# Kernel optimization log

Measured on AMD Instinct MI355X. Metric: run time of the kernel, lower is better.

The kernel has to match this reference:

```python
import jax, jax.numpy as jnp
import numpy as np

N, E = 50000, 800000
IN_C, HID, OUT_C = 100, 128, 40
LAYERS, GROUPS, CODES = 3, 3, 16
BETA = 0.98
EPS = 1e-5


def setup_inputs() -> dict:
    key = jax.random.key(0)
    ks = jax.random.split(key, 16)
    lin = lambda k, i, o: (jax.random.normal(k, (i, o), jnp.float32) / np.sqrt(i)).astype(jnp.float32)
    d = {}
    d["x"] = jax.random.normal(ks[0], (N, IN_C), jnp.float32)
    d["src"] = jax.random.randint(ks[1], (E,), 0, N, jnp.int32)
    d["dst"] = jax.random.randint(ks[2], (E,), 0, N, jnp.int32)
    # SAGEConv params: lin_l (aggregated, with bias) and lin_r (root, no bias)
    d["W0a"], d["W0r"], d["b0"] = lin(ks[3], IN_C, HID), lin(ks[4], IN_C, HID), jnp.zeros((HID,), jnp.float32)
    d["W1a"], d["W1r"], d["b1"] = lin(ks[5], HID, HID), lin(ks[6], HID, HID), jnp.zeros((HID,), jnp.float32)
    d["W2a"], d["W2r"], d["b2"] = lin(ks[7], HID, HID), lin(ks[8], HID, HID), jnp.zeros((HID,), jnp.float32)
    # BatchNorm (eval mode: running stats) for first num_layers-1 = 2 layers
    d["bn_gamma"] = jnp.ones((2, HID), jnp.float32)
    d["bn_beta"] = jnp.zeros((2, HID), jnp.float32)
    d["bn_mean"] = jnp.zeros((2, HID), jnp.float32)
    d["bn_var"] = jnp.ones((2, HID), jnp.float32)
    # Residual VQ codebooks: [layer, group, num_codes, feature]
    d["codebooks"] = 0.1 * jax.random.normal(ks[9], (LAYERS, GROUPS, CODES, HID), jnp.float32)
    d["lin_W"] = lin(ks[10], HID, OUT_C)
    d["lin_b"] = jnp.zeros((OUT_C,), jnp.float32)
    return d


def _sage_conv(h, src, dst, Wa, Wr, b):
    # mean neighbor aggregation (PyG SAGEConv, aggr='mean')
    msg = h[src]                                              # [E, d]
    agg = jax.ops.segment_sum(msg, dst, num_segments=N)       # [N, d]
    deg = jax.ops.segment_sum(jnp.ones((E,), h.dtype), dst, num_segments=N)
    agg = agg / jnp.maximum(deg, 1.0)[:, None]
    return agg @ Wa + b + h @ Wr


def _rvq(h, cb):
    # residual vector quantization over GROUPS codebooks; cb: [G, K, D]
    res, quant, ids = h, jnp.zeros_like(h), []
    for g in range(GROUPS):
        c = cb[g]                                             # [K, D]
        d2 = (jnp.sum(res * res, -1, keepdims=True)
              - 2.0 * res @ c.T + jnp.sum(c * c, -1))          # [N, K]
        idx = jnp.argmin(d2, axis=-1)
        q = c[idx]
        quant = quant + q
        res = res - q
        ids.append(idx)
    sg = jax.lax.stop_gradient
    loss = (BETA * jnp.mean((h - sg(quant)) ** 2)
            + (1.0 - BETA) * jnp.mean((sg(h) - quant) ** 2))
    return loss, jnp.stack(ids, axis=1)                        # [N, G] int


def reference(x, src, dst, W0a, W0r, b0, W1a, W1r, b1, W2a, W2r, b2,
              bn_gamma, bn_beta, bn_mean, bn_var, codebooks, lin_W, lin_b):
    Ws = [(W0a, W0r, b0), (W1a, W1r, b1), (W2a, W2r, b2)]
    h = x
    total_loss = jnp.float32(0.0)
    id_list = []
    for i in range(LAYERS - 1):
        h = _sage_conv(h, src, dst, *Ws[i])
        h = (h - bn_mean[i]) * jax.lax.rsqrt(bn_var[i] + EPS) * bn_gamma[i] + bn_beta[i]
        h = jax.nn.relu(h)                                     # dropout: eval mode (identity)
        loss, ids = _rvq(h, codebooks[i])
        total_loss = total_loss + loss
        id_list.append(ids)
    h = _sage_conv(h, src, dst, *Ws[-1])
    loss, ids = _rvq(h, codebooks[-1])
    total_loss = total_loss + loss
    id_list.append(ids)
    out = h @ lin_W + lin_b
    return out, total_loss, jnp.concatenate(id_list, axis=1)
```

## Files before the change

kernel.cpp:

```cpp
#include <hip/hip_runtime.h>

#define NN 50000
#define HID 128
#define IN_C 100
#define OUT_C 40

__global__ __launch_bounds__(256)
void hist_kernel(const int* __restrict__ dst, int* __restrict__ deg, int E) {
    int e = blockIdx.x * 256 + threadIdx.x;
    if (e < E) atomicAdd(&deg[dst[e]], 1);
}

__global__ __launch_bounds__(256)
void chunk_sum_kernel(const int* __restrict__ deg, int* __restrict__ chunk_sums, int N) {
    __shared__ int s[256];
    const int t = threadIdx.x;
    const int i = blockIdx.x * 256 + t;
    s[t] = (i < N) ? deg[i] : 0;
    __syncthreads();
    for (int o = 128; o; o >>= 1) { if (t < o) s[t] += s[t + o]; __syncthreads(); }
    if (t == 0) chunk_sums[blockIdx.x] = s[0];
}

__global__ __launch_bounds__(256)
void chunk_scan_kernel(int* __restrict__ chunk_sums, int M) {
    __shared__ int s[256];
    const int t = threadIdx.x;
    int v = (t < M) ? chunk_sums[t] : 0;
    s[t] = v;
    __syncthreads();
    for (int o = 1; o < 256; o <<= 1) {
        int x = (t >= o) ? s[t - o] : 0;
        __syncthreads();
        s[t] += x;
        __syncthreads();
    }
    if (t < M) chunk_sums[t] = s[t] - v;
}

__global__ __launch_bounds__(256)
void chunk_apply_kernel(const int* __restrict__ deg, const int* __restrict__ chunk_sums,
                        int* __restrict__ row_start, int* __restrict__ cursor, int N) {
    __shared__ int s[256];
    const int t = threadIdx.x;
    const int i = blockIdx.x * 256 + t;
    int v = (i < N) ? deg[i] : 0;
    s[t] = v;
    __syncthreads();
    for (int o = 1; o < 256; o <<= 1) {
        int x = (t >= o) ? s[t - o] : 0;
        __syncthreads();
        s[t] += x;
        __syncthreads();
    }
    if (i < N) {
        int ex = chunk_sums[blockIdx.x] + s[t] - v;
        row_start[i] = ex;
        cursor[i] = ex;
        if (i == N - 1) row_start[N] = ex + v;
    }
}

__global__ __launch_bounds__(256)
void scatter_kernel(const int* __restrict__ src, const int* __restrict__ dst,
                    int* __restrict__ cursor, int* __restrict__ csr_src, int E) {
    int e = blockIdx.x * 256 + threadIdx.x;
    if (e < E) {
        int pos = atomicAdd(&cursor[dst[e]], 1);
        csr_src[pos] = src[e];
    }
}

__global__ __launch_bounds__(128)
void prep_pack(const float* __restrict__ Wa, const float* __restrict__ Wr,
               float2* __restrict__ wp) {
    const int k = blockIdx.x, col = threadIdx.x;
    float2 v;
    v.x = Wa[(size_t)k * HID + col];
    v.y = Wr[(size_t)k * HID + col];
    wp[(size_t)k * HID + col] = v;
}

template<int K, bool HAS_BN, bool LAST>
__global__ __launch_bounds__(512, 6)
void layer_fused(const float* __restrict__ h_in,
                 const int* __restrict__ row_start, const int* __restrict__ csr_src,
                 const float2* __restrict__ wp, const float* __restrict__ b,
                 const float* __restrict__ gamma, const float* __restrict__ beta,
                 const float* __restrict__ mean, const float* __restrict__ var,
                 const float* __restrict__ cb,
                 float* __restrict__ h_out,
                 float* __restrict__ ids_out, int id_col0,
                 double* __restrict__ loss_part,
                 const float* __restrict__ lin_W, const float* __restrict__ lin_b,
                 float* __restrict__ out) {
    __shared__ double s_agg[8][HID];
    __shared__ double s_h[8][HID];
    __shared__ float s_cb[3 * 16 * HID];
    __shared__ double s_ws[8];
    const int t = threadIdx.x;
    const int w = t >> 6, lane = t & 63;
    const int n0 = blockIdx.x * 8;

    for (int idx = t; idx < 3 * 16 * HID; idx += 512) s_cb[idx] = cb[idx];

    {
        const int n = n0 + w;
        const int r0 = row_start[n], r1 = row_start[n + 1];
        const int f0 = 2 * lane;
        if (f0 < K) {
            double a0 = 0.0, a1 = 0.0, c0 = 0.0, c1 = 0.0;
            int i = r0;
            for (; i + 1 < r1; i += 2) {
                const float2 v0 = *(const float2*)(h_in + (size_t)csr_src[i] * K + f0);
                const float2 v1 = *(const float2*)(h_in + (size_t)csr_src[i + 1] * K + f0);
                a0 += (double)v0.x; a1 += (double)v0.y;
                c0 += (double)v1.x; c1 += (double)v1.y;
            }
            if (i < r1) {
                const float2 v0 = *(const float2*)(h_in + (size_t)csr_src[i] * K + f0);
                a0 += (double)v0.x; a1 += (double)v0.y;
            }
            const int deg = r1 - r0;
            const double dd = (double)(deg > 1 ? deg : 1);
            const float2 root = *(const float2*)(h_in + (size_t)n * K + f0);
            s_agg[w][f0]     = (a0 + c0) / dd;
            s_agg[w][f0 + 1] = (a1 + c1) / dd;
            s_h[w][f0]     = (double)root.x;
            s_h[w][f0 + 1] = (double)root.y;
        }
    }
    __syncthreads();

    const int col = t & 127;
    const int p4 = t >> 7;
    double accA = (double)b[col];
    double accB = accA;
#pragma unroll 4
    for (int k = 0; k < K; ++k) {
        const float2 wv = wp[(size_t)k * HID + col];
        const double wa = (double)wv.x, wr = (double)wv.y;
        accA += s_agg[p4][k] * wa + s_h[p4][k] * wr;
        accB += s_agg[p4 + 4][k] * wa + s_h[p4 + 4][k] * wr;
    }
    __syncthreads();

    {
        double vA = accA, vB = accB;
        if (HAS_BN) {
            const double scale = (double)gamma[col] / sqrt((double)var[col] + 1e-5);
            const double shift = (double)beta[col] - (double)mean[col] * scale;
            vA = vA * scale + shift; vA = vA > 0.0 ? vA : 0.0;
            vB = vB * scale + shift; vB = vB > 0.0 ? vB : 0.0;
        }
        const float fA = (float)vA, fB = (float)vB;
        h_out[(size_t)(n0 + p4) * HID + col] = fA;
        h_out[(size_t)(n0 + p4 + 4) * HID + col] = fB;
        s_agg[p4][col] = (double)fA;
        s_agg[p4 + 4][col] = (double)fB;
        if (LAST) {
            s_h[p4][col] = (double)fA;
            s_h[p4 + 4][col] = (double)fB;
        }
    }
    __syncthreads();

    {
        double* res = &s_agg[w][0];
        const int n = n0 + w;
        const int k = lane & 15, q = lane >> 4;
        const int jbase = q * 32;
        const int rot = (k + 8 * q) & 31;

        for (int g = 0; g < 3; ++g) {
            const float* c = &s_cb[(g * 16 + k) * HID];
            double r0 = res[lane], r1 = res[lane + 64];
            double pr = r0 * r0 + r1 * r1;
            pr += __shfl_xor(pr, 1, 64);
            pr += __shfl_xor(pr, 2, 64);
            pr += __shfl_xor(pr, 4, 64);
            pr += __shfl_xor(pr, 8, 64);
            pr += __shfl_xor(pr, 16, 64);
            pr += __shfl_xor(pr, 32, 64);
            const float rr32 = (float)pr;

            double cc = 0.0, dot = 0.0;
#pragma unroll
            for (int j2 = 0; j2 < 32; ++j2) {
                const int j = jbase + ((j2 + rot) & 31);
                const double cj = (double)c[j];
                cc += cj * cj;
                dot += res[j] * cj;
            }
            cc += __shfl_xor(cc, 16, 64);
            cc += __shfl_xor(cc, 32, 64);
            dot += __shfl_xor(dot, 16, 64);
            dot += __shfl_xor(dot, 32, 64);

            const float cc32 = (float)cc;
            const float rc32 = (float)dot;
            const float t1 = rr32 - 2.0f * rc32;
            const float d2 = t1 + cc32;

            float bv = d2; int bk = k;
            {
                float ov; int ok;
                ov = __shfl_xor(bv, 1, 64); ok = __shfl_xor(bk, 1, 64);
                if (ov < bv || (ov == bv && ok < bk)) { bv = ov; bk = ok; }
                ov = __shfl_xor(bv, 2, 64); ok = __shfl_xor(bk, 2, 64);
                if (ov < bv || (ov == bv && ok < bk)) { bv = ov; bk = ok; }
                ov = __shfl_xor(bv, 4, 64); ok = __shfl_xor(bk, 4, 64);
                if (ov < bv || (ov == bv && ok < bk)) { bv = ov; bk = ok; }
                ov = __shfl_xor(bv, 8, 64); ok = __shfl_xor(bk, 8, 64);
                if (ov < bv || (ov == bv && ok < bk)) { bv = ov; bk = ok; }
            }
            if (lane == 0)
                ids_out[(size_t)n * 9 + id_col0 + g] = (float)bk;

            const float* cbest = &s_cb[(g * 16 + bk) * HID];
            res[lane]      -= (double)cbest[lane];
            res[lane + 64] -= (double)cbest[lane + 64];
        }
        double r0 = res[lane], r1 = res[lane + 64];
        double wl = r0 * r0 + r1 * r1;
        wl += __shfl_xor(wl, 1, 64);
        wl += __shfl_xor(wl, 2, 64);
        wl += __shfl_xor(wl, 4, 64);
        wl += __shfl_xor(wl, 8, 64);
        wl += __shfl_xor(wl, 16, 64);
        wl += __shfl_xor(wl, 32, 64);
        if (lane == 0) s_ws[w] = wl;
    }

    if (LAST) {
        const int n = n0 + w;
        if (lane < OUT_C) {
            double acc = (double)lin_b[lane];
            for (int kk = 0; kk < HID; ++kk)
                acc += s_h[w][kk] * (double)lin_W[kk * OUT_C + lane];
            out[(size_t)n * OUT_C + lane] = (float)acc;
        }
    }

    __syncthreads();
    if (t == 0) {
        double s = 0.0;
#pragma unroll
        for (int i = 0; i < 8; i++) s += s_ws[i];
        loss_part[blockIdx.x] = s;
    }
}

__global__ __launch_bounds__(256)
void finalize_kernel(const double* __restrict__ loss_part, int M,
                     float* __restrict__ out_loss) {
    __shared__ double s[256];
    const int t = threadIdx.x;
    double v = 0.0;
    for (int i = t; i < M; i += 256) v += loss_part[i];
    s[t] = v;
    __syncthreads();
    for (int off = 128; off; off >>= 1) {
        if (t < off) s[t] += s[t + off];
        __syncthreads();
    }
    if (t == 0) out_loss[0] = (float)(s[0] / ((double)NN * (double)HID));
}

extern "C" void kernel_launch(void* const* d_in, const int* in_sizes, int n_in,
                              void* d_out, int out_size, void* d_ws, size_t ws_size,
                              hipStream_t stream) {
    const float* x    = (const float*)d_in[0];
    const int*   src  = (const int*)d_in[1];
    const int*   dst  = (const int*)d_in[2];
    const float* W0a = (const float*)d_in[3];
    const float* W0r = (const float*)d_in[4];
    const float* b0  = (const float*)d_in[5];
    const float* W1a = (const float*)d_in[6];
    const float* W1r = (const float*)d_in[7];
    const float* b1  = (const float*)d_in[8];
    const float* W2a = (const float*)d_in[9];
    const float* W2r = (const float*)d_in[10];
    const float* b2  = (const float*)d_in[11];
    const float* bn_gamma = (const float*)d_in[12];
    const float* bn_beta  = (const float*)d_in[13];
    const float* bn_mean  = (const float*)d_in[14];
    const float* bn_var   = (const float*)d_in[15];
    const float* cb    = (const float*)d_in[16];
    const float* lin_W = (const float*)d_in[17];
    const float* lin_b = (const float*)d_in[18];

    const int E = in_sizes[1];

    float* out      = (float*)d_out;
    float* out_loss = out + (size_t)NN * OUT_C;
    float* out_ids  = out_loss + 1;

    char* base = (char*)d_ws;
    size_t off = 0;
    auto alloc = [&](size_t bytes) -> void* {
        off = (off + 511) & ~(size_t)511;
        void* p = base + off;
        off += bytes;
        return p;
    };
    int* deg_i      = (int*)alloc((size_t)NN * 4);
    int* row_start  = (int*)alloc((size_t)(NN + 1) * 4);
    int* cursor     = (int*)alloc((size_t)NN * 4);
    int* csr_src    = (int*)alloc((size_t)E * 4);
    int* chunk_sums = (int*)alloc(256 * 4);
    double* loss_part = (double*)alloc((size_t)3 * 6250 * 8);
    float* h1  = (float*)alloc((size_t)NN * HID * 4);
    float* h2  = (float*)alloc((size_t)NN * HID * 4);
    float2* wp0 = (float2*)alloc((size_t)IN_C * HID * 8);
    float2* wp1 = (float2*)alloc((size_t)HID * HID * 8);
    float2* wp2 = (float2*)alloc((size_t)HID * HID * 8);

    const int cb_layer = 3 * 16 * HID;
    const int NB = NN / 8;
    const int NCHUNK = (NN + 255) / 256;

    hipMemsetAsync(deg_i, 0, NN * sizeof(int), stream);
    hist_kernel<<<(E + 255) / 256, 256, 0, stream>>>(dst, deg_i, E);
    chunk_sum_kernel<<<NCHUNK, 256, 0, stream>>>(deg_i, chunk_sums, NN);
    chunk_scan_kernel<<<1, 256, 0, stream>>>(chunk_sums, NCHUNK);
    chunk_apply_kernel<<<NCHUNK, 256, 0, stream>>>(deg_i, chunk_sums, row_start, cursor, NN);
    scatter_kernel<<<(E + 255) / 256, 256, 0, stream>>>(src, dst, cursor, csr_src, E);

    prep_pack<<<IN_C, 128, 0, stream>>>(W0a, W0r, wp0);
    prep_pack<<<HID, 128, 0, stream>>>(W1a, W1r, wp1);
    prep_pack<<<HID, 128, 0, stream>>>(W2a, W2r, wp2);

    layer_fused<IN_C, true, false><<<NB, 512, 0, stream>>>(
        x, row_start, csr_src, wp0, b0, bn_gamma, bn_beta, bn_mean, bn_var,
        cb + 0 * cb_layer, h1, out_ids, 0, loss_part, nullptr, nullptr, nullptr);

    layer_fused<HID, true, false><<<NB, 512, 0, stream>>>(
        h1, row_start, csr_src, wp1, b1,
        bn_gamma + HID, bn_beta + HID, bn_mean + HID, bn_var + HID,
        cb + 1 * cb_layer, h2, out_ids, 3, loss_part + NB, nullptr, nullptr, nullptr);

    layer_fused<HID, false, true><<<NB, 512, 0, stream>>>(
        h2, row_start, csr_src, wp2, b2, nullptr, nullptr, nullptr, nullptr,
        cb + 2 * cb_layer, h1, out_ids, 6, loss_part + 2 * NB, lin_W, lin_b, out);

    finalize_kernel<<<1, 256, 0, stream>>>(loss_part, 3 * NB, out_loss);
}
```

Before: 1.167 ms.

## Store hidden activations in double and drop weight pre-packing kernels

Intermediate hidden states h1/h2 are now kept in double rather than float, and the layer kernel is templated on the input type. The prep_pack launches are removed, so Wa and Wr are read directly as separate arrays. The neighbour gather loop is unrolled by four with eight accumulators, and the per-warp loss scratch now reuses shared s_agg. Double-precision activations double the bytes moved by the gather-heavy aggregation in layers 2 and 3, trading bandwidth for accuracy, while dropping the pack kernels saves a few launches.

```diff
diff --git a/kernel.cpp b/kernel.cpp
--- a/kernel.cpp
+++ b/kernel.cpp
@@ -71,25 +71,24 @@
     }
 }
 
-__global__ __launch_bounds__(128)
-void prep_pack(const float* __restrict__ Wa, const float* __restrict__ Wr,
-               float2* __restrict__ wp) {
-    const int k = blockIdx.x, col = threadIdx.x;
-    float2 v;
-    v.x = Wa[(size_t)k * HID + col];
-    v.y = Wr[(size_t)k * HID + col];
-    wp[(size_t)k * HID + col] = v;
-}
-
-template<int K, bool HAS_BN, bool LAST>
+__device__ __forceinline__ double2 ld2(const double* p) {
+    return *(const double2*)p;
+}
+__device__ __forceinline__ double2 ld2(const float* p) {
+    float2 v = *(const float2*)p;
+    return make_double2((double)v.x, (double)v.y);
+}
+
+template<int K, bool HAS_BN, bool LAST, typename TIN>
 __global__ __launch_bounds__(512, 6)
-void layer_fused(const float* __restrict__ h_in,
+void layer_fused(const TIN* __restrict__ h_in,
                  const int* __restrict__ row_start, const int* __restrict__ csr_src,
-                 const float2* __restrict__ wp, const float* __restrict__ b,
+                 const float* __restrict__ Wa, const float* __restrict__ Wr,
+                 const float* __restrict__ b,
                  const float* __restrict__ gamma, const float* __restrict__ beta,
                  const float* __restrict__ mean, const float* __restrict__ var,
                  const float* __restrict__ cb,
-                 float* __restrict__ h_out,
+                 double* __restrict__ h_out,
                  float* __restrict__ ids_out, int id_col0,
                  double* __restrict__ loss_part,
                  const float* __restrict__ lin_W, const float* __restrict__ lin_b,
@@ -97,7 +96,6 @@
     __shared__ double s_agg[8][HID];
     __shared__ double s_h[8][HID];
     __shared__ float s_cb[3 * 16 * HID];
-    __shared__ double s_ws[8];
     const int t = threadIdx.x;
     const int w = t >> 6, lane = t & 63;
     const int n0 = blockIdx.x * 8;
@@ -109,25 +107,27 @@
         const int r0 = row_start[n], r1 = row_start[n + 1];
         const int f0 = 2 * lane;
         if (f0 < K) {
-            double a0 = 0.0, a1 = 0.0, c0 = 0.0, c1 = 0.0;
+            double s0 = 0, s1 = 0, s2 = 0, s3 = 0, s4 = 0, s5 = 0, s6 = 0, s7 = 0;
             int i = r0;
-            for (; i + 1 < r1; i += 2) {
-                const float2 v0 = *(const float2*)(h_in + (size_t)csr_src[i] * K + f0);
-                const float2 v1 = *(const float2*)(h_in + (size_t)csr_src[i + 1] * K + f0);
-                a0 += (double)v0.x; a1 += (double)v0.y;
-                c0 += (double)v1.x; c1 += (double)v1.y;
+            for (; i + 3 < r1; i += 4) {
+                double2 v0 = ld2(h_in + (size_t)csr_src[i] * K + f0);
+                double2 v1 = ld2(h_in + (size_t)csr_src[i + 1] * K + f0);
+                double2 v2 = ld2(h_in + (size_t)csr_src[i + 2] * K + f0);
+                double2 v3 = ld2(h_in + (size_t)csr_src[i + 3] * K + f0);
+                s0 += v0.x; s1 += v0.y; s2 += v1.x; s3 += v1.y;
+                s4 += v2.x; s5 += v2.y; s6 += v3.x; s7 += v3.y;
             }
-            if (i < r1) {
-                const float2 v0 = *(const float2*)(h_in + (size_t)csr_src[i] * K + f0);
-                a0 += (double)v0.x; a1 += (double)v0.y;
+            for (; i < r1; ++i) {
+                double2 v = ld2(h_in + (size_t)csr_src[i] * K + f0);
+                s0 += v.x; s1 += v.y;
             }
             const int deg = r1 - r0;
             const double dd = (double)(deg > 1 ? deg : 1);
-            const float2 root = *(const float2*)(h_in + (size_t)n * K + f0);
-            s_agg[w][f0]     = (a0 + c0) / dd;
-            s_agg[w][f0 + 1] = (a1 + c1) / dd;
-            s_h[w][f0]     = (double)root.x;
-            s_h[w][f0 + 1] = (double)root.y;
+            const double2 root = ld2(h_in + (size_t)n * K + f0);
+            s_agg[w][f0]     = ((s0 + s2) + (s4 + s6)) / dd;
+            s_agg[w][f0 + 1] = ((s1 + s3) + (s5 + s7)) / dd;
+            s_h[w][f0]     = root.x;
+            s_h[w][f0 + 1] = root.y;
         }
     }
     __syncthreads();
@@ -138,8 +138,8 @@
     double accB = accA;
 #pragma unroll 4
     for (int k = 0; k < K; ++k) {
-        const float2 wv = wp[(size_t)k * HID + col];
-        const double wa = (double)wv.x, wr = (double)wv.y;
+        const double wa = (double)Wa[(size_t)k * HID + col];
+        const double wr = (double)Wr[(size_t)k * HID + col];
         accA += s_agg[p4][k] * wa + s_h[p4][k] * wr;
         accB += s_agg[p4 + 4][k] * wa + s_h[p4 + 4][k] * wr;
     }
@@ -153,18 +153,18 @@
             vA = vA * scale + shift; vA = vA > 0.0 ? vA : 0.0;
             vB = vB * scale + shift; vB = vB > 0.0 ? vB : 0.0;
         }
-        const float fA = (float)vA, fB = (float)vB;
-        h_out[(size_t)(n0 + p4) * HID + col] = fA;
-        h_out[(size_t)(n0 + p4 + 4) * HID + col] = fB;
-        s_agg[p4][col] = (double)fA;
-        s_agg[p4 + 4][col] = (double)fB;
+        h_out[(size_t)(n0 + p4) * HID + col] = vA;
+        h_out[(size_t)(n0 + p4 + 4) * HID + col] = vB;
+        s_agg[p4][col] = vA;
+        s_agg[p4 + 4][col] = vB;
         if (LAST) {
-            s_h[p4][col] = (double)fA;
-            s_h[p4 + 4][col] = (double)fB;
-        }
-    }
-    __syncthreads();
-
+            s_h[p4][col] = vA;
+            s_h[p4 + 4][col] = vB;
+        }
+    }
+    __syncthreads();
+
+    double wl;
     {
         double* res = &s_agg[w][0];
         const int n = n0 + w;
@@ -222,15 +222,17 @@
             res[lane + 64] -= (double)cbest[lane + 64];
         }
         double r0 = res[lane], r1 = res[lane + 64];
-        double wl = r0 * r0 + r1 * r1;
+        wl = r0 * r0 + r1 * r1;
         wl += __shfl_xor(wl, 1, 64);
         wl += __shfl_xor(wl, 2, 64);
         wl += __shfl_xor(wl, 4, 64);
         wl += __shfl_xor(wl, 8, 64);
         wl += __shfl_xor(wl, 16, 64);
         wl += __shfl_xor(wl, 32, 64);
-        if (lane == 0) s_ws[w] = wl;
-    }
+    }
+
+    __syncthreads();
+    if (lane == 0) s_agg[0][w] = wl;
 
     if (LAST) {
         const int n = n0 + w;
@@ -246,7 +248,7 @@
     if (t == 0) {
         double s = 0.0;
 #pragma unroll
-        for (int i = 0; i < 8; i++) s += s_ws[i];
+        for (int i = 0; i < 8; i++) s += s_agg[0][i];
         loss_part[blockIdx.x] = s;
     }
 }
@@ -310,11 +312,8 @@
     int* csr_src    = (int*)alloc((size_t)E * 4);
     int* chunk_sums = (int*)alloc(256 * 4);
     double* loss_part = (double*)alloc((size_t)3 * 6250 * 8);
-    float* h1  = (float*)alloc((size_t)NN * HID * 4);
-    float* h2  = (float*)alloc((size_t)NN * HID * 4);
-    float2* wp0 = (float2*)alloc((size_t)IN_C * HID * 8);
-    float2* wp1 = (float2*)alloc((size_t)HID * HID * 8);
-    float2* wp2 = (float2*)alloc((size_t)HID * HID * 8);
+    double* h1 = (double*)alloc((size_t)NN * HID * 8);
+    double* h2 = (double*)alloc((size_t)NN * HID * 8);
 
     const int cb_layer = 3 * 16 * HID;
     const int NB = NN / 8;
@@ -327,21 +326,17 @@
     chunk_apply_kernel<<<NCHUNK, 256, 0, stream>>>(deg_i, chunk_sums, row_start, cursor, NN);
     scatter_kernel<<<(E + 255) / 256, 256, 0, stream>>>(src, dst, cursor, csr_src, E);
 
-    prep_pack<<<IN_C, 128, 0, stream>>>(W0a, W0r, wp0);
-    prep_pack<<<HID, 128, 0, stream>>>(W1a, W1r, wp1);
-    prep_pack<<<HID, 128, 0, stream>>>(W2a, W2r, wp2);
-
-    layer_fused<IN_C, true, false><<<NB, 512, 0, stream>>>(
-        x, row_start, csr_src, wp0, b0, bn_gamma, bn_beta, bn_mean, bn_var,
+    layer_fused<IN_C, true, false, float><<<NB, 512, 0, stream>>>(
+        x, row_start, csr_src, W0a, W0r, b0, bn_gamma, bn_beta, bn_mean, bn_var,
         cb + 0 * cb_layer, h1, out_ids, 0, loss_part, nullptr, nullptr, nullptr);
 
-    layer_fused<HID, true, false><<<NB, 512, 0, stream>>>(
-        h1, row_start, csr_src, wp1, b1,
+    layer_fused<HID, true, false, double><<<NB, 512, 0, stream>>>(
+        h1, row_start, csr_src, W1a, W1r, b1,
         bn_gamma + HID, bn_beta + HID, bn_mean + HID, bn_var + HID,
         cb + 1 * cb_layer, h2, out_ids, 3, loss_part + NB, nullptr, nullptr, nullptr);
 
-    layer_fused<HID, false, true><<<NB, 512, 0, stream>>>(
-        h2, row_start, csr_src, wp2, b2, nullptr, nullptr, nullptr, nullptr,
+    layer_fused<HID, false, true, double><<<NB, 512, 0, stream>>>(
+        h2, row_start, csr_src, W2a, W2r, b2, nullptr, nullptr, nullptr, nullptr,
         cb + 2 * cb_layer, h1, out_ids, 6, loss_part + 2 * NB, lin_W, lin_b, out);
 
     finalize_kernel<<<1, 256, 0, stream>>>(loss_part, 3 * NB, out_loss);
```

After: 1.132 ms. 1.03x faster.
